# Kernel optimization log

Measured on AMD Instinct MI355X. Metric: run time of the kernel, lower is better.

## Reference

```python
import jax, jax.numpy as jnp
import numpy as np

N = 100000      # nodes
E = 3200000     # edges
F_IN = 64       # num_input_features
HID = 3         # hardcoded hidden width in GCN
F_OUT = 256     # gcn_output_features
F_TR = 512      # transformer_feature_size


def setup_inputs() -> dict:
    key = jax.random.key(0)
    ks = jax.random.split(key, 12)
    x = jax.random.normal(ks[0], (N, F_IN), dtype=jnp.float32)
    edge_index = jax.random.randint(ks[1], (2, E), 0, N, dtype=jnp.int64)
    s = 0.05
    # ChebConv1 (K=2): two weight mats [in,out] + bias
    W0a = jax.random.normal(ks[2], (F_IN, HID), jnp.float32) * s
    W1a = jax.random.normal(ks[3], (F_IN, HID), jnp.float32) * s
    b1 = jax.random.normal(ks[4], (HID,), jnp.float32) * s
    # ChebConv2 (K=2)
    W0b = jax.random.normal(ks[5], (HID, F_OUT), jnp.float32) * s
    W1b = jax.random.normal(ks[6], (HID, F_OUT), jnp.float32) * s
    b2 = jax.random.normal(ks[7], (F_OUT,), jnp.float32) * s
    # final Linear
    Wl = jax.random.normal(ks[8], (F_OUT, F_TR), jnp.float32) * s
    bl = jax.random.normal(ks[9], (F_TR,), jnp.float32) * s
    return {"x": x, "edge_index": edge_index, "W0a": W0a, "W1a": W1a,
            "b1": b1, "W0b": W0b, "W1b": W1b, "b2": b2, "Wl": Wl, "bl": bl}


def _cheb_norm(edge_index, num_nodes):
    # PyG ChebConv.__norm__ with sym normalization, lambda_max=2.0:
    # L_hat = 2L/2 - I = -D^{-1/2} A D^{-1/2} (diagonal cancels to 0).
    src, dst = edge_index[0], edge_index[1]
    w = jnp.where(src != dst, 1.0, 0.0).astype(jnp.float32)  # remove_self_loops
    deg = jnp.zeros((num_nodes,), jnp.float32).at[src].add(w)
    dinv = jnp.where(deg > 0, jax.lax.rsqrt(jnp.maximum(deg, 1.0)), 0.0)
    return -dinv[src] * w * dinv[dst]  # [E]


def _cheb_conv(x, edge_index, norm, W0, W1, b):
    # K=2 Chebyshev: Tx0 = x, Tx1 = L_hat @ x (scatter-add over edges)
    src, dst = edge_index[0], edge_index[1]
    Tx1 = jnp.zeros_like(x).at[dst].add(norm[:, None] * x[src])
    return x @ W0 + Tx1 @ W1 + b


def reference(x, edge_index, W0a, W1a, b1, W0b, W1b, b2, Wl, bl):
    norm = _cheb_norm(edge_index, x.shape[0])
    h = jax.nn.relu(_cheb_conv(x, edge_index, norm, W0a, W1a, b1))
    h = jax.nn.relu(_cheb_conv(h, edge_index, norm, W0b, W1b, b2))
    return h @ Wl + bl
```

## Files before the change

### kernel.cpp

```cpp
#include <hip/hip_runtime.h>
#include <hip/hip_bf16.h>


#define MAXNB 1024
#define BSH 7
#define BSZ 128
#define SRC_BITS 20
#define SRC_MASK ((1u << SRC_BITS) - 1u)
#define EPB 16384

typedef __attribute__((ext_vector_type(8))) short short8;
typedef __attribute__((ext_vector_type(4))) float f32x4;

static __device__ inline unsigned short f2bf(float f) {
    union { float f; unsigned u; } v; v.f = f;
    unsigned r = (v.u + 0x7fffu + ((v.u >> 16) & 1u)) >> 16;
    return (unsigned short)r;
}

__global__ __launch_bounds__(256) void k_hist(const int* __restrict__ ei, int E, int NB,
                                              unsigned* __restrict__ subcurD,
                                              unsigned* __restrict__ subcurS,
                                              unsigned* __restrict__ baseD,
                                              unsigned* __restrict__ baseS) {
    __shared__ unsigned hD[MAXNB], hS[MAXNB];
    int t = threadIdx.x, blk = blockIdx.x;
    for (int i = t; i < NB; i += 256) { hD[i] = 0u; hS[i] = 0u; }
    __syncthreads();
    int e0 = blk * EPB, e1 = min(e0 + EPB, E);
    for (int e = e0 + t; e < e1; e += 256) {
        int s = ei[e], d = ei[E + e];
        if (s != d) {
            atomicAdd(&hD[d >> BSH], 1u);
            atomicAdd(&hS[s >> BSH], 1u);
        }
    }
    __syncthreads();
    unsigned* bD = baseD + (size_t)blk * NB;
    unsigned* bS = baseS + (size_t)blk * NB;
    for (int i = t; i < NB; i += 256) {
        unsigned h = hD[i];
        if (h) bD[i] = atomicAdd(&subcurD[i], h);
        h = hS[i];
        if (h) bS[i] = atomicAdd(&subcurS[i], h);
    }
}

__global__ __launch_bounds__(1024) void k_scan(const unsigned* __restrict__ totD,
                                               const unsigned* __restrict__ totS,
                                               unsigned* __restrict__ startD,
                                               unsigned* __restrict__ startS, int NB) {
    __shared__ unsigned a[MAXNB], b[MAXNB];
    int t = threadIdx.x;
    for (int i = t; i < NB; i += 1024) a[i] = totD[i];
    __syncthreads();
    unsigned* s = a; unsigned* d = b;
    for (int off = 1; off < NB; off <<= 1) {
        for (int i = t; i < NB; i += 1024)
            d[i] = s[i] + (i >= off ? s[i - off] : 0u);
        __syncthreads();
        unsigned* tmp = s; s = d; d = tmp;
    }
    for (int i = t; i < NB; i += 1024)
        startD[i] = (i == 0) ? 0u : s[i - 1];
    if (t == 0) startD[NB] = s[NB - 1];
    __syncthreads();
    for (int i = t; i < NB; i += 1024) a[i] = totS[i];
    __syncthreads();
    s = a; d = b;
    for (int off = 1; off < NB; off <<= 1) {
        for (int i = t; i < NB; i += 1024)
            d[i] = s[i] + (i >= off ? s[i - off] : 0u);
        __syncthreads();
        unsigned* tmp = s; s = d; d = tmp;
    }
    for (int i = t; i < NB; i += 1024)
        startS[i] = (i == 0) ? 0u : s[i - 1];
    if (t == 0) startS[NB] = s[NB - 1];
}

__global__ __launch_bounds__(256) void k_place(const int* __restrict__ ei, int E, int NB,
                                               const unsigned* __restrict__ startD,
                                               const unsigned* __restrict__ startS,
                                               const unsigned* __restrict__ baseD,
                                               const unsigned* __restrict__ baseS,
                                               unsigned* __restrict__ dstbin,
                                               unsigned char* __restrict__ srcbin) {
    __shared__ unsigned oD[MAXNB], oS[MAXNB], cD[MAXNB], cS[MAXNB];
    int t = threadIdx.x, blk = blockIdx.x;
    const unsigned* bD = baseD + (size_t)blk * NB;
    const unsigned* bS = baseS + (size_t)blk * NB;
    for (int i = t; i < NB; i += 256) {
        oD[i] = startD[i] + bD[i];
        oS[i] = startS[i] + bS[i];
        cD[i] = 0u; cS[i] = 0u;
    }
    __syncthreads();
    int e0 = blk * EPB, e1 = min(e0 + EPB, E);
    for (int e = e0 + t; e < e1; e += 256) {
        int s = ei[e], d = ei[E + e];
        if (s != d) {
            int bk = d >> BSH;
            unsigned pos = oD[bk] + atomicAdd(&cD[bk], 1u);
            dstbin[pos] = ((unsigned)(d & (BSZ - 1)) << SRC_BITS) | (unsigned)s;
            int bs = s >> BSH;
            unsigned ps = oS[bs] + atomicAdd(&cS[bs], 1u);
            srcbin[ps] = (unsigned char)(s & (BSZ - 1));
        }
    }
}

__global__ __launch_bounds__(256) void k_sort2(const unsigned* __restrict__ dstbin,
                                               const unsigned* __restrict__ startD,
                                               unsigned* __restrict__ dsorted,
                                               unsigned* __restrict__ nodeoff, int N) {
    __shared__ unsigned cnt[BSZ], tmp[BSZ], cur[BSZ];
    int t = threadIdx.x, b = blockIdx.x;
    if (t < BSZ) cnt[t] = 0u;
    __syncthreads();
    unsigned i0 = startD[b], i1 = startD[b + 1];
    for (unsigned e = i0 + t; e < i1; e += 256)
        atomicAdd(&cnt[dstbin[e] >> SRC_BITS], 1u);
    __syncthreads();
    for (int off = 1; off < BSZ; off <<= 1) {
        if (t < BSZ) tmp[t] = cnt[t] + (t >= off ? cnt[t - off] : 0u);
        __syncthreads();
        if (t < BSZ) cnt[t] = tmp[t];
        __syncthreads();
    }
    if (t <= BSZ) {
        unsigned ex = (t == 0) ? 0u : cnt[t - 1];
        int idx = b * BSZ + t;
        if (idx <= N) nodeoff[idx] = i0 + ex;
        if (t < BSZ) cur[t] = ex;
    }
    __syncthreads();
    for (unsigned e = i0 + t; e < i1; e += 256) {
        unsigned p = dstbin[e];
        unsigned pos = i0 + atomicAdd(&cur[p >> SRC_BITS], 1u);
        dsorted[pos] = p & SRC_MASK;
    }
}

__global__ __launch_bounds__(256) void k_deggemm(
    const unsigned char* __restrict__ srcbin, const unsigned* __restrict__ startS,
    const float* __restrict__ x, const float* __restrict__ W0a,
    const float* __restrict__ W1a, float* __restrict__ dinv,
    float4* __restrict__ a3v, float4* __restrict__ y3v, int N) {
    __shared__ unsigned cnt[4][BSZ];
    __shared__ float w0[192], w1[192];
    __shared__ float dl[BSZ];
    int t = threadIdx.x, b = blockIdx.x;
    if (t < 192) { w0[t] = W0a[t]; w1[t] = W1a[t]; }
    for (int i = t; i < 4 * BSZ; i += 256) ((unsigned*)cnt)[i] = 0u;
    __syncthreads();
    unsigned i0 = startS[b], i1 = startS[b + 1];
    int rep = t & 3;
    for (unsigned i = i0 + t; i < i1; i += 256) atomicAdd(&cnt[rep][srcbin[i]], 1u);
    __syncthreads();
    if (t < BSZ) {
        unsigned c = cnt[0][t] + cnt[1][t] + cnt[2][t] + cnt[3][t];
        float dv = c ? rsqrtf((float)c) : 0.f;
        dl[t] = dv;
        int g = b * BSZ + t;
        if (g < N) dinv[g] = dv;
    }
    __syncthreads();
    int q = t & 3;
#pragma unroll
    for (int pass = 0; pass < 2; pass++) {
        int nn = (t >> 2) + pass * 64;
        int node = b * BSZ + nn;
        float acc[6] = {0.f, 0.f, 0.f, 0.f, 0.f, 0.f};
        if (node < N) {
            const float4* xr = (const float4*)(x + (size_t)node * 64 + q * 16);
#pragma unroll
            for (int i = 0; i < 4; i++) {
                float4 v = xr[i];
                float xs[4] = {v.x, v.y, v.z, v.w};
#pragma unroll
                for (int c = 0; c < 4; c++) {
                    int f = q * 16 + i * 4 + c;
                    float xi = xs[c];
                    acc[0] += xi * w0[f * 3 + 0];
                    acc[1] += xi * w0[f * 3 + 1];
                    acc[2] += xi * w0[f * 3 + 2];
                    acc[3] += xi * w1[f * 3 + 0];
                    acc[4] += xi * w1[f * 3 + 1];
                    acc[5] += xi * w1[f * 3 + 2];
                }
            }
        }
#pragma unroll
        for (int m = 1; m < 4; m <<= 1)
#pragma unroll
            for (int j = 0; j < 6; j++) acc[j] += __shfl_xor(acc[j], m, 64);
        if (q == 0 && node < N) {
            a3v[node] = make_float4(acc[0], acc[1], acc[2], 0.f);
            y3v[node] = make_float4(acc[3], acc[4], acc[5], dl[nn]);
        }
    }
}

__global__ __launch_bounds__(512) void k_tgather(
    const unsigned* __restrict__ dsorted, const unsigned* __restrict__ nodeoff,
    const float4* __restrict__ v4, const float* __restrict__ dinv,
    const float4* __restrict__ a3v, const float* __restrict__ b1,
    float4* __restrict__ outv, int N, int phase) {
    int t = threadIdx.x;
    int g = t >> 3, q = t & 7;
    int node = blockIdx.x * 64 + g;
    if (node >= N) return;
    float dv = dinv[node];
    unsigned o0 = nodeoff[node], o1 = nodeoff[node + 1];
    float s0 = 0.f, s1 = 0.f, s2 = 0.f;
    for (unsigned e = o0 + q; e < o1; e += 8) {
        float4 v = v4[dsorted[e]];
        float nm = -v.w * dv;
        s0 += nm * v.x; s1 += nm * v.y; s2 += nm * v.z;
    }
#pragma unroll
    for (int m = 1; m < 8; m <<= 1) {
        s0 += __shfl_xor(s0, m, 64);
        s1 += __shfl_xor(s1, m, 64);
        s2 += __shfl_xor(s2, m, 64);
    }
    if (q == 0) {
        if (phase == 1) {
            float4 a = a3v[node];
            outv[node] = make_float4(fmaxf(s0 + a.x + b1[0], 0.f),
                                     fmaxf(s1 + a.y + b1[1], 0.f),
                                     fmaxf(s2 + a.z + b1[2], 0.f), dv);
        } else {
            outv[node] = make_float4(s0, s1, s2, 0.f);
        }
    }
}

__global__ __launch_bounds__(256) void k_prep(const float* __restrict__ Wl,
                                              unsigned short* __restrict__ WlT) {
    __shared__ float tile[32][33];
    int t = threadIdx.x, tx = t & 31, ty = t >> 5;
    int kb = (blockIdx.x & 7) * 32;
    int cb = (blockIdx.x >> 3) * 32;
#pragma unroll
    for (int r = 0; r < 4; r++) {
        int k = kb + ty + r * 8;
        tile[ty + r * 8][tx] = Wl[(size_t)k * 512 + cb + tx];
    }
    __syncthreads();
#pragma unroll
    for (int r = 0; r < 4; r++) {
        int c = cb + ty + r * 8;
        WlT[(size_t)c * 256 + kb + tx] = f2bf(tile[tx][ty + r * 8]);
    }
}

__global__ __launch_bounds__(256) void k_final_mfma(
    const float4* __restrict__ h1v, const float4* __restrict__ t2r,
    const float* __restrict__ W0b, const float* __restrict__ W1b,
    const float* __restrict__ b2, const unsigned short* __restrict__ WlT,
    const float* __restrict__ bl, float* __restrict__ out, int N) {
    __shared__ unsigned short h2s[64 * 256];
    __shared__ float4 u4[64][2];
    char* h2b = (char*)h2s;
    int t = threadIdx.x, b = blockIdx.x;
    int n0 = b * 64;

    if (t < 64) {
        int g = n0 + t;
        u4[t][0] = (g < N) ? h1v[g] : make_float4(0.f, 0.f, 0.f, 0.f);
    } else if (t < 128) {
        int g = n0 + t - 64;
        u4[t - 64][1] = (g < N) ? t2r[g] : make_float4(0.f, 0.f, 0.f, 0.f);
    }
    __syncthreads();

    {
        int k0 = (t & 127) * 2;
        int rh = (t >> 7) * 32;
        float w00a = W0b[k0],       w00b = W0b[k0 + 1];
        float w01a = W0b[256 + k0], w01b = W0b[256 + k0 + 1];
        float w02a = W0b[512 + k0], w02b = W0b[512 + k0 + 1];
        float w10a = W1b[k0],       w10b = W1b[k0 + 1];
        float w11a = W1b[256 + k0], w11b = W1b[256 + k0 + 1];
        float w12a = W1b[512 + k0], w12b = W1b[512 + k0 + 1];
        float bka = b2[k0], bkb = b2[k0 + 1];
        int kbyte = k0 * 2;
#pragma unroll
        for (int r = 0; r < 32; r++) {
            int rr = rh + r;
            float4 h = u4[rr][0];
            float4 v = u4[rr][1];
            float za = bka + h.x * w00a + h.y * w01a + h.z * w02a
                           + v.x * w10a + v.y * w11a + v.z * w12a;
            float zb = bkb + h.x * w00b + h.y * w01b + h.z * w02b
                           + v.x * w10b + v.y * w11b + v.z * w12b;
            za = fmaxf(za, 0.f); zb = fmaxf(zb, 0.f);
            unsigned pk = ((unsigned)f2bf(zb) << 16) | (unsigned)f2bf(za);
            int byte = rr * 512 + (kbyte ^ ((rr & 7) << 4));
            *(unsigned*)(h2b + byte) = pk;
        }
    }
    __syncthreads();

    int w = t >> 6, l = t & 63;
    int col0 = w * 128;
    int lrow = l & 15, lkb = (l >> 4) * 8, cq = (l >> 4) * 4;

#pragma unroll
    for (int ch = 0; ch < 2; ch++) {
        int cb0 = col0 + ch * 64;
        f32x4 acc[4][4];
#pragma unroll
        for (int rt = 0; rt < 4; rt++)
#pragma unroll
            for (int ct = 0; ct < 4; ct++) acc[rt][ct] = (f32x4)0.f;

#pragma unroll
        for (int ks = 0; ks < 8; ks++) {
            int kel = ks * 32 + lkb;
            short8 af[4];
#pragma unroll
            for (int rt = 0; rt < 4; rt++) {
                int r = rt * 16 + lrow;
                int byte = r * 512 + ((kel * 2) ^ ((r & 7) << 4));
                af[rt] = *(const short8*)(h2b + byte);
            }
            short8 bf[4];
#pragma unroll
            for (int ct = 0; ct < 4; ct++) {
                int c = cb0 + ct * 16 + lrow;
                bf[ct] = *(const short8*)(WlT + (size_t)c * 256 + kel);
            }
#pragma unroll
            for (int rt = 0; rt < 4; rt++)
#pragma unroll
                for (int ct = 0; ct < 4; ct++)
                    acc[rt][ct] = __builtin_amdgcn_mfma_f32_16x16x32_bf16(
                        bf[ct], af[rt], acc[rt][ct], 0, 0, 0);
        }

        float4 blv[4];
#pragma unroll
        for (int ct = 0; ct < 4; ct++)
            blv[ct] = *(const float4*)(bl + cb0 + ct * 16 + cq);
#pragma unroll
        for (int rt = 0; rt < 4; rt++) {
            int row = n0 + rt * 16 + lrow;
            if (row < N) {
                float* orow = out + (size_t)row * 512 + cb0 + cq;
#pragma unroll
                for (int ct = 0; ct < 4; ct++) {
                    f32x4 a = acc[rt][ct];
                    float4 st = make_float4(a[0] + blv[ct].x, a[1] + blv[ct].y,
                                            a[2] + blv[ct].z, a[3] + blv[ct].w);
                    *(float4*)(orow + ct * 16) = st;
                }
            }
        }
    }
}

extern "C" void kernel_launch(void* const* d_in, const int* in_sizes, int n_in,
                              void* d_out, int out_size, void* d_ws, size_t ws_size,
                              hipStream_t stream) {
    const float* x   = (const float*)d_in[0];
    const int*   ei  = (const int*)d_in[1];
    const float* W0a = (const float*)d_in[2];
    const float* W1a = (const float*)d_in[3];
    const float* b1  = (const float*)d_in[4];
    const float* W0b = (const float*)d_in[5];
    const float* W1b = (const float*)d_in[6];
    const float* b2  = (const float*)d_in[7];
    const float* Wl  = (const float*)d_in[8];
    const float* bl  = (const float*)d_in[9];
    float* out = (float*)d_out;

    const int N = in_sizes[0] / 64;
    const int E = in_sizes[1] / 2;
    const int NB = (N + BSZ - 1) >> BSH;
    const int CB = (E + EPB - 1) / EPB;
    const int NB64 = (N + 63) / 64;

    char* base = (char*)d_ws;
    size_t off = 0;
    auto alloc = [&](size_t bytes) {
        void* p = base + off;
        off = (off + bytes + 255) & ~(size_t)255;
        return p;
    };
    unsigned* subcurD = (unsigned*)alloc(MAXNB * 4);
    unsigned* subcurS = (unsigned*)alloc(MAXNB * 4);
    unsigned* startD  = (unsigned*)alloc((MAXNB + 1) * 4);
    unsigned* startS  = (unsigned*)alloc((MAXNB + 1) * 4);
    unsigned* baseD   = (unsigned*)alloc((size_t)CB * NB * 4);
    unsigned* baseS   = (unsigned*)alloc((size_t)CB * NB * 4);
    unsigned* dstbin  = (unsigned*)alloc((size_t)E * 4);
    unsigned* dsorted = (unsigned*)alloc((size_t)E * 4);
    unsigned* nodeoff = (unsigned*)alloc((size_t)(N + 1) * 4);
    unsigned char* srcbin = (unsigned char*)alloc((size_t)E);
    float* dinv = (float*)alloc((size_t)N * 4);
    float* a3v  = (float*)alloc((size_t)N * 16);
    float* y3v  = (float*)alloc((size_t)N * 16);
    float* h1v  = (float*)alloc((size_t)N * 16);
    float* t2r  = (float*)alloc((size_t)N * 16);
    unsigned short* WlT = (unsigned short*)alloc(512 * 256 * 2);

    hipMemsetAsync(subcurD, 0, 2 * MAXNB * 4, stream);

    k_prep<<<128, 256, 0, stream>>>(Wl, WlT);
    k_hist<<<CB, 256, 0, stream>>>(ei, E, NB, subcurD, subcurS, baseD, baseS);
    k_scan<<<1, 1024, 0, stream>>>(subcurD, subcurS, startD, startS, NB);
    k_place<<<CB, 256, 0, stream>>>(ei, E, NB, startD, startS, baseD, baseS,
                                    dstbin, srcbin);
    k_sort2<<<NB, 256, 0, stream>>>(dstbin, startD, dsorted, nodeoff, N);
    k_deggemm<<<NB, 256, 0, stream>>>(srcbin, startS, x, W0a, W1a, dinv,
                                      (float4*)a3v, (float4*)y3v, N);
    k_tgather<<<NB64, 512, 0, stream>>>(dsorted, nodeoff, (const float4*)y3v, dinv,
                                        (const float4*)a3v, b1, (float4*)h1v, N, 1);
    k_tgather<<<NB64, 512, 0, stream>>>(dsorted, nodeoff, (const float4*)h1v, dinv,
                                        (const float4*)a3v, b1, (float4*)t2r, N, 2);
    k_final_mfma<<<NB64, 256, 0, stream>>>(
        (const float4*)h1v, (const float4*)t2r, W0b, W1b, b2, WlT, bl, out, N);
}
```

Measured before the change: 256.5 us.

## Fuse sort and degree kernels, fold memset into prep, widen hist/place blocks

```diff
diff --git a/kernel.cpp b/kernel.cpp
--- a/kernel.cpp
+++ b/kernel.cpp
@@ -18,17 +18,41 @@
     return (unsigned short)r;
 }
 
-__global__ __launch_bounds__(256) void k_hist(const int* __restrict__ ei, int E, int NB,
+__global__ __launch_bounds__(256) void k_prep(const float* __restrict__ Wl,
+                                              unsigned short* __restrict__ WlT,
                                               unsigned* __restrict__ subcurD,
-                                              unsigned* __restrict__ subcurS,
-                                              unsigned* __restrict__ baseD,
-                                              unsigned* __restrict__ baseS) {
+                                              unsigned* __restrict__ subcurS) {
+    __shared__ float tile[32][33];
+    int t = threadIdx.x, tx = t & 31, ty = t >> 5;
+    if (blockIdx.x == 0) {
+        for (int i = t; i < MAXNB; i += 256) { subcurD[i] = 0u; subcurS[i] = 0u; }
+    }
+    int kb = (blockIdx.x & 7) * 32;
+    int cb = (blockIdx.x >> 3) * 32;
+#pragma unroll
+    for (int r = 0; r < 4; r++) {
+        int k = kb + ty + r * 8;
+        tile[ty + r * 8][tx] = Wl[(size_t)k * 512 + cb + tx];
+    }
+    __syncthreads();
+#pragma unroll
+    for (int r = 0; r < 4; r++) {
+        int c = cb + ty + r * 8;
+        WlT[(size_t)c * 256 + kb + tx] = f2bf(tile[tx][ty + r * 8]);
+    }
+}
+
+__global__ __launch_bounds__(1024) void k_hist(const int* __restrict__ ei, int E, int NB,
+                                               unsigned* __restrict__ subcurD,
+                                               unsigned* __restrict__ subcurS,
+                                               unsigned* __restrict__ baseD,
+                                               unsigned* __restrict__ baseS) {
     __shared__ unsigned hD[MAXNB], hS[MAXNB];
     int t = threadIdx.x, blk = blockIdx.x;
-    for (int i = t; i < NB; i += 256) { hD[i] = 0u; hS[i] = 0u; }
+    for (int i = t; i < NB; i += 1024) { hD[i] = 0u; hS[i] = 0u; }
     __syncthreads();
     int e0 = blk * EPB, e1 = min(e0 + EPB, E);
-    for (int e = e0 + t; e < e1; e += 256) {
+    for (int e = e0 + t; e < e1; e += 1024) {
         int s = ei[e], d = ei[E + e];
         if (s != d) {
             atomicAdd(&hD[d >> BSH], 1u);
@@ -38,7 +62,7 @@
     __syncthreads();
     unsigned* bD = baseD + (size_t)blk * NB;
     unsigned* bS = baseS + (size_t)blk * NB;
-    for (int i = t; i < NB; i += 256) {
+    for (int i = t; i < NB; i += 1024) {
         unsigned h = hD[i];
         if (h) bD[i] = atomicAdd(&subcurD[i], h);
         h = hS[i];
@@ -79,25 +103,25 @@
     if (t == 0) startS[NB] = s[NB - 1];
 }
 
-__global__ __launch_bounds__(256) void k_place(const int* __restrict__ ei, int E, int NB,
-                                               const unsigned* __restrict__ startD,
-                                               const unsigned* __restrict__ startS,
-                                               const unsigned* __restrict__ baseD,
-                                               const unsigned* __restrict__ baseS,
-                                               unsigned* __restrict__ dstbin,
-                                               unsigned char* __restrict__ srcbin) {
+__global__ __launch_bounds__(1024) void k_place(const int* __restrict__ ei, int E, int NB,
+                                                const unsigned* __restrict__ startD,
+                                                const unsigned* __restrict__ startS,
+                                                const unsigned* __restrict__ baseD,
+                                                const unsigned* __restrict__ baseS,
+                                                unsigned* __restrict__ dstbin,
+                                                unsigned char* __restrict__ srcbin) {
     __shared__ unsigned oD[MAXNB], oS[MAXNB], cD[MAXNB], cS[MAXNB];
     int t = threadIdx.x, blk = blockIdx.x;
     const unsigned* bD = baseD + (size_t)blk * NB;
     const unsigned* bS = baseS + (size_t)blk * NB;
-    for (int i = t; i < NB; i += 256) {
+    for (int i = t; i < NB; i += 1024) {
         oD[i] = startD[i] + bD[i];
         oS[i] = startS[i] + bS[i];
         cD[i] = 0u; cS[i] = 0u;
     }
     __syncthreads();
     int e0 = blk * EPB, e1 = min(e0 + EPB, E);
-    for (int e = e0 + t; e < e1; e += 256) {
+    for (int e = e0 + t; e < e1; e += 1024) {
         int s = ei[e], d = ei[E + e];
         if (s != d) {
             int bk = d >> BSH;
@@ -110,17 +134,28 @@
     }
 }
 
-__global__ __launch_bounds__(256) void k_sort2(const unsigned* __restrict__ dstbin,
-                                               const unsigned* __restrict__ startD,
-                                               unsigned* __restrict__ dsorted,
-                                               unsigned* __restrict__ nodeoff, int N) {
+__global__ __launch_bounds__(256) void k_sortdeg(
+    const unsigned* __restrict__ dstbin, const unsigned* __restrict__ startD,
+    unsigned* __restrict__ dsorted, unsigned* __restrict__ nodeoff,
+    const unsigned char* __restrict__ srcbin, const unsigned* __restrict__ startS,
+    const float* __restrict__ x, const float* __restrict__ W0a,
+    const float* __restrict__ W1a, float* __restrict__ dinv,
+    float4* __restrict__ a3v, float4* __restrict__ y3v, int N) {
     __shared__ unsigned cnt[BSZ], tmp[BSZ], cur[BSZ];
+    __shared__ unsigned cnt4[4][BSZ];
+    __shared__ float w0[192], w1[192];
+    __shared__ float dl[BSZ];
     int t = threadIdx.x, b = blockIdx.x;
+    if (t < 192) { w0[t] = W0a[t]; w1[t] = W1a[t]; }
     if (t < BSZ) cnt[t] = 0u;
-    __syncthreads();
-    unsigned i0 = startD[b], i1 = startD[b + 1];
-    for (unsigned e = i0 + t; e < i1; e += 256)
+    for (int i = t; i < 4 * BSZ; i += 256) ((unsigned*)cnt4)[i] = 0u;
+    __syncthreads();
+    unsigned d0 = startD[b], d1 = startD[b + 1];
+    for (unsigned e = d0 + t; e < d1; e += 256)
         atomicAdd(&cnt[dstbin[e] >> SRC_BITS], 1u);
+    unsigned s0 = startS[b], s1 = startS[b + 1];
+    int rep = t & 3;
+    for (unsigned i = s0 + t; i < s1; i += 256) atomicAdd(&cnt4[rep][srcbin[i]], 1u);
     __syncthreads();
     for (int off = 1; off < BSZ; off <<= 1) {
         if (t < BSZ) tmp[t] = cnt[t] + (t >= off ? cnt[t - off] : 0u);
@@ -131,35 +166,17 @@
     if (t <= BSZ) {
         unsigned ex = (t == 0) ? 0u : cnt[t - 1];
         int idx = b * BSZ + t;
-        if (idx <= N) nodeoff[idx] = i0 + ex;
+        if (idx <= N) nodeoff[idx] = d0 + ex;
         if (t < BSZ) cur[t] = ex;
     }
     __syncthreads();
-    for (unsigned e = i0 + t; e < i1; e += 256) {
+    for (unsigned e = d0 + t; e < d1; e += 256) {
         unsigned p = dstbin[e];
-        unsigned pos = i0 + atomicAdd(&cur[p >> SRC_BITS], 1u);
+        unsigned pos = d0 + atomicAdd(&cur[p >> SRC_BITS], 1u);
         dsorted[pos] = p & SRC_MASK;
     }
-}
-
-__global__ __launch_bounds__(256) void k_deggemm(
-    const unsigned char* __restrict__ srcbin, const unsigned* __restrict__ startS,
-    const float* __restrict__ x, const float* __restrict__ W0a,
-    const float* __restrict__ W1a, float* __restrict__ dinv,
-    float4* __restrict__ a3v, float4* __restrict__ y3v, int N) {
-    __shared__ unsigned cnt[4][BSZ];
-    __shared__ float w0[192], w1[192];
-    __shared__ float dl[BSZ];
-    int t = threadIdx.x, b = blockIdx.x;
-    if (t < 192) { w0[t] = W0a[t]; w1[t] = W1a[t]; }
-    for (int i = t; i < 4 * BSZ; i += 256) ((unsigned*)cnt)[i] = 0u;
-    __syncthreads();
-    unsigned i0 = startS[b], i1 = startS[b + 1];
-    int rep = t & 3;
-    for (unsigned i = i0 + t; i < i1; i += 256) atomicAdd(&cnt[rep][srcbin[i]], 1u);
-    __syncthreads();
     if (t < BSZ) {
-        unsigned c = cnt[0][t] + cnt[1][t] + cnt[2][t] + cnt[3][t];
+        unsigned c = cnt4[0][t] + cnt4[1][t] + cnt4[2][t] + cnt4[3][t];
         float dv = c ? rsqrtf((float)c) : 0.f;
         dl[t] = dv;
         int g = b * BSZ + t;
@@ -237,25 +254,6 @@
     }
 }
 
-__global__ __launch_bounds__(256) void k_prep(const float* __restrict__ Wl,
-                                              unsigned short* __restrict__ WlT) {
-    __shared__ float tile[32][33];
-    int t = threadIdx.x, tx = t & 31, ty = t >> 5;
-    int kb = (blockIdx.x & 7) * 32;
-    int cb = (blockIdx.x >> 3) * 32;
-#pragma unroll
-    for (int r = 0; r < 4; r++) {
-        int k = kb + ty + r * 8;
-        tile[ty + r * 8][tx] = Wl[(size_t)k * 512 + cb + tx];
-    }
-    __syncthreads();
-#pragma unroll
-    for (int r = 0; r < 4; r++) {
-        int c = cb + ty + r * 8;
-        WlT[(size_t)c * 256 + kb + tx] = f2bf(tile[tx][ty + r * 8]);
-    }
-}
-
 __global__ __launch_bounds__(256) void k_final_mfma(
     const float4* __restrict__ h1v, const float4* __restrict__ t2r,
     const float* __restrict__ W0b, const float* __restrict__ W1b,
@@ -341,10 +339,10 @@
                         bf[ct], af[rt], acc[rt][ct], 0, 0, 0);
         }
 
-        float4 blv[4];
+        f32x4 blv[4];
 #pragma unroll
         for (int ct = 0; ct < 4; ct++)
-            blv[ct] = *(const float4*)(bl + cb0 + ct * 16 + cq);
+            blv[ct] = *(const f32x4*)(bl + cb0 + ct * 16 + cq);
 #pragma unroll
         for (int rt = 0; rt < 4; rt++) {
             int row = n0 + rt * 16 + lrow;
@@ -352,10 +350,8 @@
                 float* orow = out + (size_t)row * 512 + cb0 + cq;
 #pragma unroll
                 for (int ct = 0; ct < 4; ct++) {
-                    f32x4 a = acc[rt][ct];
-                    float4 st = make_float4(a[0] + blv[ct].x, a[1] + blv[ct].y,
-                                            a[2] + blv[ct].z, a[3] + blv[ct].w);
-                    *(float4*)(orow + ct * 16) = st;
+                    f32x4 sv = acc[rt][ct] + blv[ct];
+                    __builtin_nontemporal_store(sv, (f32x4*)(orow + ct * 16));
                 }
             }
         }
@@ -407,15 +403,13 @@
     float* t2r  = (float*)alloc((size_t)N * 16);
     unsigned short* WlT = (unsigned short*)alloc(512 * 256 * 2);
 
-    hipMemsetAsync(subcurD, 0, 2 * MAXNB * 4, stream);
-
-    k_prep<<<128, 256, 0, stream>>>(Wl, WlT);
-    k_hist<<<CB, 256, 0, stream>>>(ei, E, NB, subcurD, subcurS, baseD, baseS);
+    k_prep<<<128, 256, 0, stream>>>(Wl, WlT, subcurD, subcurS);
+    k_hist<<<CB, 1024, 0, stream>>>(ei, E, NB, subcurD, subcurS, baseD, baseS);
     k_scan<<<1, 1024, 0, stream>>>(subcurD, subcurS, startD, startS, NB);
-    k_place<<<CB, 256, 0, stream>>>(ei, E, NB, startD, startS, baseD, baseS,
-                                    dstbin, srcbin);
-    k_sort2<<<NB, 256, 0, stream>>>(dstbin, startD, dsorted, nodeoff, N);
-    k_deggemm<<<NB, 256, 0, stream>>>(srcbin, startS, x, W0a, W1a, dinv,
+    k_place<<<CB, 1024, 0, stream>>>(ei, E, NB, startD, startS, baseD, baseS,
+                                     dstbin, srcbin);
+    k_sortdeg<<<NB, 256, 0, stream>>>(dstbin, startD, dsorted, nodeoff,
+                                      srcbin, startS, x, W0a, W1a, dinv,
                                       (float4*)a3v, (float4*)y3v, N);
     k_tgather<<<NB64, 512, 0, stream>>>(dsorted, nodeoff, (const float4*)y3v, dinv,
                                         (const float4*)a3v, b1, (float4*)h1v, N, 1);
```

Result: faster. 234.2 us (-8.7%).
